# Optimization experiments

Hardware: AMD Instinct MI355X
Metric: run time of the kernel (lower is better)

The kernel has to match this reference:

```python
import jax, jax.numpy as jnp
import numpy as np

HID = 3584      # hidden_size
NQ = 16         # num query heads
NKV = 8         # num kv heads
D = 256         # head_dim
SCALE = 256.0 ** -0.5   # query_pre_attn_scalar ** -0.5
CAP = 50.0      # attn_logits_soft_cap
WINDOW = 2048   # interleaved sliding window (even layer)
THETA = 10000.0
B, S = 1, 4096


def _rope(x, positions):
    """Neox-style RoPE. x: [B,S,N,D], positions: [B,S] int."""
    half = D // 2
    inv_freq = 1.0 / (THETA ** (jnp.arange(half, dtype=jnp.float32) / half))
    freqs = positions.astype(jnp.float32)[:, :, None] * inv_freq  # [B,S,half]
    cos = jnp.cos(freqs)[:, :, None, :]  # [B,S,1,half]
    sin = jnp.sin(freqs)[:, :, None, :]
    x1, x2 = x[..., :half], x[..., half:]
    return jnp.concatenate([x1 * cos - x2 * sin, x2 * cos + x1 * sin], axis=-1)


def setup_inputs() -> dict:
    key = jax.random.key(0)
    k1, k2, k3 = jax.random.split(key, 3)
    positions = jnp.broadcast_to(jnp.arange(S, dtype=jnp.int64)[None, :], (B, S))
    hidden_states = jax.random.normal(k1, (B, S, HID), dtype=jnp.float32)
    # scale weights ~ 1/sqrt(fan_in) so activations are O(1)
    w_qkv = jax.random.normal(k2, ((NQ + 2 * NKV) * D, HID), dtype=jnp.float32) * (HID ** -0.5)
    w_o = jax.random.normal(k3, (HID, NQ * D), dtype=jnp.float32) * ((NQ * D) ** -0.5)
    return {"positions": positions, "hidden_states": hidden_states, "w_qkv": w_qkv, "w_o": w_o}


def reference(positions, hidden_states, w_qkv, w_o):
    q_size, kv_size = NQ * D, NKV * D
    qkv = jnp.einsum('bsh,oh->bso', hidden_states, w_qkv)
    q = qkv[..., :q_size].reshape(B, S, NQ, D)
    k = qkv[..., q_size:q_size + kv_size].reshape(B, S, NKV, D)
    v = qkv[..., q_size + kv_size:].reshape(B, S, NKV, D)
    q = _rope(q, positions)
    k = _rope(k, positions)
    # GQA: repeat kv heads to match query heads
    g = NQ // NKV
    k = jnp.repeat(k, g, axis=2)  # [B,S,NQ,D]
    v = jnp.repeat(v, g, axis=2)
    scores = jnp.einsum('bqhd,bkhd->bhqk', q, k) * SCALE
    # Gemma2 logit soft-capping
    scores = CAP * jnp.tanh(scores / CAP)
    i = jnp.arange(S)[:, None]
    j = jnp.arange(S)[None, :]
    mask = (j <= i) & (i - j < WINDOW)  # causal + sliding window
    scores = jnp.where(mask, scores, -1e30)
    probs = jax.nn.softmax(scores, axis=-1)
    attn = jnp.einsum('bhqk,bkhd->bqhd', probs, v).reshape(B, S, NQ * D)
    return jnp.einsum('bso,ho->bsh', attn, w_o)
```

## Files before the change

kernel.cpp:

```cpp
#include <hip/hip_runtime.h>
#include <hip/hip_bf16.h>

typedef __bf16 bf16_t;
typedef __bf16 bf16x8 __attribute__((ext_vector_type(8)));
typedef float f32x4 __attribute__((ext_vector_type(4)));

#define HIDDEN 3584
#define NQH 16
#define NKVH 8
#define DH 256
#define SEQ 4096
#define QKV_COLS 8192
#define Q_SIZE 4096
#define KV_SIZE 2048
#define WINDOW 2048
#define SCALE_F 0.0625f
#define CAP_F 50.0f
#define SM_MAX 12.0f

__device__ __forceinline__ float fast_tanh(float x) {
  return 1.0f - 2.0f / (__expf(2.0f * x) + 1.0f);
}

__device__ __forceinline__ void gload16(const bf16_t* g, bf16_t* l) {
  __builtin_amdgcn_global_load_lds((__attribute__((address_space(1))) void*)g,
                                   (__attribute__((address_space(3))) void*)l, 16, 0, 0);
}

__global__ __launch_bounds__(256) void cvt_f32_to_bf16(const float* __restrict__ src,
                                                       bf16_t* __restrict__ dst, long n8) {
  long i = (long)blockIdx.x * 256 + threadIdx.x;
  if (i >= n8) return;
  const float4* s4 = (const float4*)src;
  float4 a = s4[i * 2];
  float4 b = s4[i * 2 + 1];
  bf16x8 o;
  o[0] = (bf16_t)a.x; o[1] = (bf16_t)a.y; o[2] = (bf16_t)a.z; o[3] = (bf16_t)a.w;
  o[4] = (bf16_t)b.x; o[5] = (bf16_t)b.y; o[6] = (bf16_t)b.z; o[7] = (bf16_t)b.w;
  *(bf16x8*)(dst + i * 8) = o;
}

#define TILE(T, WSTR, STAGE)                                                                \
  {                                                                                         \
    char* buf = lds + ((T) & 3) * 32768;                                                    \
    bf16x8 af[8], b0, b1, b2, b3;                                                           \
    _Pragma("unroll")                                                                       \
    for (int i = 0; i < 8; ++i) af[i] = *(const bf16x8*)(buf + aoff + i * 1024);            \
    b0 = *(const bf16x8*)(buf + boff);                                                      \
    b1 = *(const bf16x8*)(buf + boff + 1024);                                               \
    if (STAGE) {                                                                            \
      char* d = lds + (((T) + 3) & 3) * 32768;                                              \
      gload16(sA0 + ((T) + 3) * 32, (bf16_t*)(d + sdst0));                                  \
      gload16(sA1 + ((T) + 3) * 32, (bf16_t*)(d + 8192 + sdst0));                           \
    }                                                                                       \
    __builtin_amdgcn_s_setprio(1);                                                          \
    _Pragma("unroll")                                                                       \
    for (int i = 0; i < 8; ++i) {                                                           \
      acc[i][0] = __builtin_amdgcn_mfma_f32_16x16x32_bf16(af[i], b0, acc[i][0], 0, 0, 0);   \
      acc[i][1] = __builtin_amdgcn_mfma_f32_16x16x32_bf16(af[i], b1, acc[i][1], 0, 0, 0);   \
    }                                                                                       \
    __builtin_amdgcn_s_setprio(0);                                                          \
    __builtin_amdgcn_s_barrier();                                                           \
    b2 = *(const bf16x8*)(buf + boff + 2048);                                               \
    b3 = *(const bf16x8*)(buf + boff + 3072);                                               \
    if (STAGE) {                                                                            \
      char* d = lds + (((T) + 3) & 3) * 32768;                                              \
      gload16(sB0 + ((T) + 3) * 32, (bf16_t*)(d + 16384 + sdst0));                          \
      gload16(sB1 + ((T) + 3) * 32, (bf16_t*)(d + 24576 + sdst0));                          \
    }                                                                                       \
    __builtin_amdgcn_s_setprio(1);                                                          \
    _Pragma("unroll")                                                                       \
    for (int i = 0; i < 8; ++i) {                                                           \
      acc[i][2] = __builtin_amdgcn_mfma_f32_16x16x32_bf16(af[i], b2, acc[i][2], 0, 0, 0);   \
      acc[i][3] = __builtin_amdgcn_mfma_f32_16x16x32_bf16(af[i], b3, acc[i][3], 0, 0, 0);   \
    }                                                                                       \
    __builtin_amdgcn_s_setprio(0);                                                          \
    asm volatile("s_waitcnt vmcnt(" WSTR ")" ::: "memory");                                 \
    __builtin_amdgcn_s_barrier();                                                           \
  }

template <int K, bool OUT_BF16>
__global__ __launch_bounds__(512, 2) void gemm_bt(const bf16_t* __restrict__ A,
                                                  const bf16_t* __restrict__ B,
                                                  void* __restrict__ Cout, int N) {
  constexpr int NT = K / 32;
  __shared__ char lds[4 * 32768];
  int tid = threadIdx.x;
  int lane = tid & 63, w = tid >> 6;
  int wm = w >> 2, wn = w & 3;
  int r16 = lane & 15, g = lane >> 4;
  int bid = blockIdx.x;
  long bm = (long)((bid & 7) * 2 + ((bid >> 3) & 1)) * 256;
  long bn = (long)(bid >> 4) * 256;
  int ro = r16 >> 1;
  int asl = ((g + ((r16 & 1) << 2)) ^ ro) << 4;
  int aoff = wm * 8192 + ro * 128 + asl;
  int boff = 16384 + wn * 4096 + ro * 128 + asl;
  int slr = lane >> 3;
  int lc = (lane & 7) ^ slr;
  int kc8 = (lc & 3) * 8;
  long mr0 = (long)(w * 8 + slr) * 2 + (lc >> 2);
  long mr1 = mr0 + 128;
  const bf16_t* sA0 = A + (bm + mr0) * K + kc8;
  const bf16_t* sA1 = A + (bm + mr1) * K + kc8;
  const bf16_t* sB0 = B + (bn + mr0) * K + kc8;
  const bf16_t* sB1 = B + (bn + mr1) * K + kc8;
  int sdst0 = w * 1024;
  f32x4 acc[8][4] = {};
#pragma unroll
  for (int u = 0; u < 3; ++u) {
    char* d = lds + u * 32768;
    gload16(sA0 + u * 32, (bf16_t*)(d + sdst0));
    gload16(sA1 + u * 32, (bf16_t*)(d + 8192 + sdst0));
    gload16(sB0 + u * 32, (bf16_t*)(d + 16384 + sdst0));
    gload16(sB1 + u * 32, (bf16_t*)(d + 24576 + sdst0));
  }
  asm volatile("s_waitcnt vmcnt(8)" ::: "memory");
  __builtin_amdgcn_s_barrier();
  int t = 0;
  for (; t < NT - 3; ++t) TILE(t, "8", true);
  TILE(t, "4", false); ++t;
  TILE(t, "0", false); ++t;
  TILE(t, "0", false);
#pragma unroll
  for (int i = 0; i < 8; ++i)
#pragma unroll
    for (int j = 0; j < 4; ++j)
#pragma unroll
      for (int r = 0; r < 4; ++r) {
        long row = bm + wm * 128 + i * 16 + g * 4 + r;
        long col = bn + wn * 64 + j * 16 + r16;
        if (OUT_BF16) ((bf16_t*)Cout)[row * N + col] = (bf16_t)acc[i][j][r];
        else          ((float*)Cout)[row * N + col]  = acc[i][j][r];
      }
}

__global__ __launch_bounds__(256) void rope_kernel(bf16_t* __restrict__ qkv) {
  long idx = (long)blockIdx.x * 256 + threadIdx.x;
  int i = (int)(idx & 127);
  long rem = idx >> 7;
  int head = (int)(rem % 24);
  int s = (int)(rem / 24);
  int base = head < NQH ? head * DH : Q_SIZE + (head - NQH) * DH;
  long p1 = (long)s * QKV_COLS + base + i;
  long p2 = p1 + 128;
  float x1 = (float)qkv[p1], x2 = (float)qkv[p2];
  float inv_freq = exp2f((float)i * -0.10381025296522976f);
  float fr = (float)s * inv_freq;
  float sn, cs;
  sincosf(fr, &sn, &cs);
  qkv[p1] = (bf16_t)(x1 * cs - x2 * sn);
  qkv[p2] = (bf16_t)(x2 * cs + x1 * sn);
}

__global__ __launch_bounds__(256) void vtrans_kernel(const bf16_t* __restrict__ qkv,
                                                     bf16_t* __restrict__ vt) {
  __shared__ bf16_t tile[64][72];
  int t = threadIdx.x;
  long s0 = (long)blockIdx.x * 64;
  long c0 = (long)blockIdx.y * 64;
#pragma unroll
  for (int it = 0; it < 2; ++it) {
    int u = t + it * 256;
    int sr = u >> 3, ch = u & 7;
    bf16x8 v = *(const bf16x8*)&qkv[(s0 + sr) * QKV_COLS + (Q_SIZE + KV_SIZE) + c0 + ch * 8];
    *(bf16x8*)&tile[sr][ch * 8] = v;
  }
  __syncthreads();
#pragma unroll
  for (int it = 0; it < 2; ++it) {
    int u = t + it * 256;
    int cr = u >> 3, ch = u & 7;
    bf16x8 o;
#pragma unroll
    for (int j = 0; j < 8; ++j) o[j] = tile[ch * 8 + j][cr];
    *(bf16x8*)&vt[(c0 + cr) * SEQ + s0 + ch * 8] = o;
  }
}

__global__ __launch_bounds__(512, 2) void attn_kernel(const bf16_t* __restrict__ qkv,
                                                      const bf16_t* __restrict__ vt,
                                                      bf16_t* __restrict__ attn_out) {
  __shared__ bf16_t Ks[64 * 256];
  __shared__ bf16_t Vs[256 * 64];
  __shared__ bf16_t Pl[8 * 1024];
  int t = threadIdx.x;
  int lane = t & 63, w = t >> 6;
  int r16 = lane & 15, g = lane >> 4;
  int bid = blockIdx.x;
  int swz = (bid & 7) * 64 + (bid >> 3);
  int h = swz >> 5;
  int qb = swz & 31;
  int kvh = h >> 1;
  int qw = qb * 128 + w * 16;
  bf16x8 qf[8];
  long qoff = (long)(qw + r16) * QKV_COLS + h * DH + g * 8;
#pragma unroll
  for (int kk = 0; kk < 8; ++kk) qf[kk] = *(const bf16x8*)&qkv[qoff + kk * 32];
  f32x4 acc[16] = {};
  float lsum[4] = {};
  int lrK = lane >> 5, slK = lane & 31;
  int lrV = lane >> 3, slV = lane & 7;
  const bf16_t* kg = qkv + Q_SIZE + (long)kvh * DH;
  const bf16_t* vg = vt + (long)kvh * DH * SEQ;
  bf16_t* ksl = Ks + w * 2048;
  bf16_t* vsl = Vs + w * 2048;
  bf16_t* pw = Pl + w * 1024;
  int t0 = qb * 128 - (WINDOW - 1);
  t0 = t0 > 0 ? (t0 >> 6) : 0;
  int t1 = (qb * 128 + 128) >> 6;
  int qlo = qw, qhi = qw + 15;
  for (int tt = t0; tt < t1; ++tt) {
    int kb = tt * 64;
    const bf16_t* kgb = kg + (long)kb * QKV_COLS;
    const bf16_t* vgb = vg + kb;
#pragma unroll
    for (int c = 0; c < 4; ++c) {
      int rowk = w * 8 + c * 2 + lrK;
      gload16(kgb + rowk * QKV_COLS + ((slK ^ (rowk & 7)) * 8), ksl + c * 512);
      int rowv = w * 32 + c * 8 + lrV;
      gload16(vgb + rowv * SEQ + ((slV ^ (rowv & 7)) * 8), vsl + c * 512);
    }
    __syncthreads();
    bool active = !(kb > qhi || kb + 63 < qlo - (WINDOW - 1));
    if (active) {
      bool full = (kb + 63 <= qlo) && (qhi - kb <= WINDOW - 1);
      f32x4 sc[4] = {};
#pragma unroll
      for (int kk = 0; kk < 8; ++kk) {
        int slot = (kk * 4 + g) ^ (r16 & 7);
#pragma unroll
        for (int c = 0; c < 4; ++c) {
          bf16x8 kf = *(const bf16x8*)&Ks[(c * 16 + r16) * 256 + slot * 8];
          sc[c] = __builtin_amdgcn_mfma_f32_16x16x32_bf16(qf[kk], kf, sc[c], 0, 0, 0);
        }
      }
#pragma unroll
      for (int c = 0; c < 4; ++c)
#pragma unroll
        for (int r = 0; r < 4; ++r) {
          float s = sc[c][r];
          float v = CAP_F * fast_tanh(s * (SCALE_F / CAP_F));
          if (!full) {
            int q = qw + g * 4 + r;
            int k = kb + c * 16 + r16;
            if (!((k <= q) && (q - k < WINDOW))) v = -1e30f;
          }
          bf16_t pb = (bf16_t)__expf(v - SM_MAX);
          lsum[r] += (float)pb;
          int prow = g * 4 + r;
          int pbyte = prow * 128 + ((c * 32 + r16 * 2) ^ ((prow & 7) << 4));
          *(bf16_t*)((char*)pw + pbyte) = pb;
        }
      bf16x8 pa[2];
#pragma unroll
      for (int pk = 0; pk < 2; ++pk) {
        int pb = r16 * 128 + ((pk * 64 + g * 16) ^ ((r16 & 7) << 4));
        pa[pk] = *(const bf16x8*)((const char*)pw + pb);
      }
#pragma unroll
      for (int dt = 0; dt < 16; ++dt)
#pragma unroll
        for (int pk = 0; pk < 2; ++pk) {
          bf16x8 vf = *(const bf16x8*)&Vs[(dt * 16 + r16) * 64 + (((pk * 4 + g) ^ (r16 & 7)) * 8)];
          acc[dt] = __builtin_amdgcn_mfma_f32_16x16x32_bf16(pa[pk], vf, acc[dt], 0, 0, 0);
        }
    }
    __syncthreads();
  }
  float inv[4];
#pragma unroll
  for (int r = 0; r < 4; ++r) {
    float s = lsum[r];
    s += __shfl_xor(s, 1);
    s += __shfl_xor(s, 2);
    s += __shfl_xor(s, 4);
    s += __shfl_xor(s, 8);
    inv[r] = 1.0f / s;
  }
#pragma unroll
  for (int dt = 0; dt < 16; ++dt)
#pragma unroll
    for (int r = 0; r < 4; ++r) {
      long row = qw + g * 4 + r;
      attn_out[row * Q_SIZE + h * DH + dt * 16 + r16] = (bf16_t)(acc[dt][r] * inv[r]);
    }
}

extern "C" void kernel_launch(void* const* d_in, const int* in_sizes, int n_in,
                              void* d_out, int out_size, void* d_ws, size_t ws_size,
                              hipStream_t stream) {
  const float* hid_f  = (const float*)d_in[1];
  const float* wqkv_f = (const float*)d_in[2];
  const float* wo_f   = (const float*)d_in[3];
  float* out = (float*)d_out;
  char* ws = (char*)d_ws;
  bf16_t* qkv    = (bf16_t*)(ws);
  bf16_t* wo_b   = (bf16_t*)(ws + 67108864);
  bf16_t* hid_b  = (bf16_t*)(ws + 96468992);
  bf16_t* wqkv_b = (bf16_t*)(ws + 125829120);
  bf16_t* attn_b = (bf16_t*)(ws + 96468992);
  bf16_t* vt     = (bf16_t*)(ws + 130023424);

  cvt_f32_to_bf16<<<7168, 256, 0, stream>>>(hid_f, hid_b, 14680064 / 8);
  cvt_f32_to_bf16<<<14336, 256, 0, stream>>>(wqkv_f, wqkv_b, 29360128 / 8);
  cvt_f32_to_bf16<<<7168, 256, 0, stream>>>(wo_f, wo_b, 14680064 / 8);
  gemm_bt<HIDDEN, true><<<512, 512, 0, stream>>>(hid_b, wqkv_b, qkv, QKV_COLS);
  rope_kernel<<<49152, 256, 0, stream>>>(qkv);
  vtrans_kernel<<<dim3(64, 32), 256, 0, stream>>>(qkv, vt);
  attn_kernel<<<512, 512, 0, stream>>>(qkv, vt, attn_b);
  gemm_bt<Q_SIZE, false><<<224, 512, 0, stream>>>(attn_b, wo_b, out, HIDDEN);
}
```

Before: 678.8 us.

## Double-buffer K/V tiles, fold softcap into exp, and raise MFMA wave priority

K and V tiles now go into two LDS buffers. The next tile's async global-to-LDS load is issued before computing on the current one, and the loop keeps a single barrier per iteration. The soft-capped softmax is rewritten algebraically as exp(38 - 100/(e+1)), so the separate tanh and exponential steps collapse into one exp, one reciprocal and one exp, with masking done by zeroing p. s_setprio is raised around both MFMA loops. Doubling K/V LDS raises usage to about 144KB per block, which likely cuts resident blocks per CU and works against the intended load/compute overlap.

```diff
diff --git a/kernel.cpp b/kernel.cpp
--- a/kernel.cpp
+++ b/kernel.cpp
@@ -2,6 +2,7 @@
 #include <hip/hip_bf16.h>
 
 typedef __bf16 bf16_t;
+typedef __bf16 bf16x4 __attribute__((ext_vector_type(4)));
 typedef __bf16 bf16x8 __attribute__((ext_vector_type(8)));
 typedef float f32x4 __attribute__((ext_vector_type(4)));
 
@@ -16,11 +17,6 @@
 #define WINDOW 2048
 #define SCALE_F 0.0625f
 #define CAP_F 50.0f
-#define SM_MAX 12.0f
-
-__device__ __forceinline__ float fast_tanh(float x) {
-  return 1.0f - 2.0f / (__expf(2.0f * x) + 1.0f);
-}
 
 __device__ __forceinline__ void gload16(const bf16_t* g, bf16_t* l) {
   __builtin_amdgcn_global_load_lds((__attribute__((address_space(1))) void*)g,
@@ -181,11 +177,11 @@
 __global__ __launch_bounds__(512, 2) void attn_kernel(const bf16_t* __restrict__ qkv,
                                                       const bf16_t* __restrict__ vt,
                                                       bf16_t* __restrict__ attn_out) {
-  __shared__ bf16_t Ks[64 * 256];
-  __shared__ bf16_t Vs[256 * 64];
+  __shared__ bf16_t Kb[2][64 * 256];
+  __shared__ bf16_t Vb[2][256 * 64];
   __shared__ bf16_t Pl[8 * 1024];
-  int t = threadIdx.x;
-  int lane = t & 63, w = t >> 6;
+  int tid = threadIdx.x;
+  int lane = tid & 63, w = tid >> 6;
   int r16 = lane & 15, g = lane >> 4;
   int bid = blockIdx.x;
   int swz = (bid & 7) * 64 + (bid >> 3);
@@ -199,58 +195,67 @@
   for (int kk = 0; kk < 8; ++kk) qf[kk] = *(const bf16x8*)&qkv[qoff + kk * 32];
   f32x4 acc[16] = {};
   float lsum[4] = {};
-  int lrK = lane >> 5, slK = lane & 31;
-  int lrV = lane >> 3, slV = lane & 7;
   const bf16_t* kg = qkv + Q_SIZE + (long)kvh * DH;
   const bf16_t* vg = vt + (long)kvh * DH * SEQ;
-  bf16_t* ksl = Ks + w * 2048;
-  bf16_t* vsl = Vs + w * 2048;
   bf16_t* pw = Pl + w * 1024;
-  int t0 = qb * 128 - (WINDOW - 1);
-  t0 = t0 > 0 ? (t0 >> 6) : 0;
-  int t1 = (qb * 128 + 128) >> 6;
+  int lo = qb * 128 - (WINDOW - 1);
+  int t0 = lo > 0 ? (lo >> 6) : 0;
+  int t1 = qb * 2 + 2;
   int qlo = qw, qhi = qw + 15;
+
+#define ATTN_STAGE(TT)                                                                   \
+  {                                                                                      \
+    int b_ = (TT) & 1;                                                                   \
+    int kb_ = (TT) * 64;                                                                 \
+    _Pragma("unroll")                                                                    \
+    for (int c = 0; c < 4; ++c) {                                                        \
+      int rowk = w * 8 + c * 2 + (lane >> 5);                                            \
+      gload16(kg + (long)(kb_ + rowk) * QKV_COLS + (((lane & 31) ^ (rowk & 7)) * 8),     \
+              &Kb[b_][w * 2048 + c * 512]);                                              \
+      int rowv = w * 32 + c * 8 + (lane >> 3);                                           \
+      gload16(vg + (long)rowv * SEQ + kb_ + (((lane & 7) ^ (rowv & 7)) * 8),             \
+              &Vb[b_][w * 2048 + c * 512]);                                              \
+    }                                                                                    \
+  }
+
+  ATTN_STAGE(t0);
+  __syncthreads();
   for (int tt = t0; tt < t1; ++tt) {
+    if (tt + 1 < t1) ATTN_STAGE(tt + 1);
+    int b = tt & 1;
     int kb = tt * 64;
-    const bf16_t* kgb = kg + (long)kb * QKV_COLS;
-    const bf16_t* vgb = vg + kb;
-#pragma unroll
-    for (int c = 0; c < 4; ++c) {
-      int rowk = w * 8 + c * 2 + lrK;
-      gload16(kgb + rowk * QKV_COLS + ((slK ^ (rowk & 7)) * 8), ksl + c * 512);
-      int rowv = w * 32 + c * 8 + lrV;
-      gload16(vgb + rowv * SEQ + ((slV ^ (rowv & 7)) * 8), vsl + c * 512);
-    }
-    __syncthreads();
     bool active = !(kb > qhi || kb + 63 < qlo - (WINDOW - 1));
     if (active) {
       bool full = (kb + 63 <= qlo) && (qhi - kb <= WINDOW - 1);
       f32x4 sc[4] = {};
+      __builtin_amdgcn_s_setprio(1);
 #pragma unroll
       for (int kk = 0; kk < 8; ++kk) {
-        int slot = (kk * 4 + g) ^ (r16 & 7);
+        int sl = ((kk * 4 + g) ^ (r16 & 7)) * 8;
 #pragma unroll
         for (int c = 0; c < 4; ++c) {
-          bf16x8 kf = *(const bf16x8*)&Ks[(c * 16 + r16) * 256 + slot * 8];
+          bf16x8 kf = *(const bf16x8*)&Kb[b][(c * 16 + r16) * 256 + sl];
           sc[c] = __builtin_amdgcn_mfma_f32_16x16x32_bf16(qf[kk], kf, sc[c], 0, 0, 0);
         }
       }
+      __builtin_amdgcn_s_setprio(0);
 #pragma unroll
       for (int c = 0; c < 4; ++c)
 #pragma unroll
         for (int r = 0; r < 4; ++r) {
           float s = sc[c][r];
-          float v = CAP_F * fast_tanh(s * (SCALE_F / CAP_F));
+          float e = __expf(s * (2.0f * SCALE_F / CAP_F));
+          float rr = __builtin_amdgcn_rcpf(e + 1.0f);
+          float p = __expf(fmaf(-100.0f, rr, 38.0f));
           if (!full) {
             int q = qw + g * 4 + r;
             int k = kb + c * 16 + r16;
-            if (!((k <= q) && (q - k < WINDOW))) v = -1e30f;
+            p = ((k <= q) && (q - k < WINDOW)) ? p : 0.0f;
           }
-          bf16_t pb = (bf16_t)__expf(v - SM_MAX);
-          lsum[r] += (float)pb;
+          lsum[r] += p;
           int prow = g * 4 + r;
           int pbyte = prow * 128 + ((c * 32 + r16 * 2) ^ ((prow & 7) << 4));
-          *(bf16_t*)((char*)pw + pbyte) = pb;
+          *(bf16_t*)((char*)pw + pbyte) = (bf16_t)p;
         }
       bf16x8 pa[2];
 #pragma unroll
@@ -258,13 +263,16 @@
         int pb = r16 * 128 + ((pk * 64 + g * 16) ^ ((r16 & 7) << 4));
         pa[pk] = *(const bf16x8*)((const char*)pw + pb);
       }
-#pragma unroll
-      for (int dt = 0; dt < 16; ++dt)
-#pragma unroll
-        for (int pk = 0; pk < 2; ++pk) {
-          bf16x8 vf = *(const bf16x8*)&Vs[(dt * 16 + r16) * 64 + (((pk * 4 + g) ^ (r16 & 7)) * 8)];
-          acc[dt] = __builtin_amdgcn_mfma_f32_16x16x32_bf16(pa[pk], vf, acc[dt], 0, 0, 0);
-        }
+      __builtin_amdgcn_s_setprio(1);
+#pragma unroll
+      for (int dt = 0; dt < 16; ++dt) {
+        int vrow = (dt * 16 + r16) * 64;
+        bf16x8 vf0 = *(const bf16x8*)&Vb[b][vrow + ((g ^ (r16 & 7)) * 8)];
+        acc[dt] = __builtin_amdgcn_mfma_f32_16x16x32_bf16(pa[0], vf0, acc[dt], 0, 0, 0);
+        bf16x8 vf1 = *(const bf16x8*)&Vb[b][vrow + (((4 + g) ^ (r16 & 7)) * 8)];
+        acc[dt] = __builtin_amdgcn_mfma_f32_16x16x32_bf16(pa[1], vf1, acc[dt], 0, 0, 0);
+      }
+      __builtin_amdgcn_s_setprio(0);
     }
     __syncthreads();
   }
```

After: 607.1 us. -10.6%, faster.
